# Kernel tuning notes

Measured on AMD Instinct MI355X. Metric: run time of the kernel, lower is better.

The kernel has to match this reference:

```python
import jax, jax.numpy as jnp
import numpy as np

LEVEL_SHAPES = ((100, 100), (50, 50), (25, 25))  # (H, W) per feature level
B, S, D, H, L, P, FFN = 2, 13125, 256, 8, 3, 4, 1024
Dh = D // H


def setup_inputs() -> dict:
    key = jax.random.key(0)
    ks = jax.random.split(key, 24)

    def rn(k, shape, s=0.02):
        return jax.random.normal(k, shape, jnp.float32) * s

    starts = np.cumsum([0] + [h * w for h, w in LEVEL_SHAPES])[:-1]
    return {
        "x": jax.random.normal(ks[0], (B, S, D), jnp.float32),
        "pos_embed": jax.random.normal(ks[1], (B, S, D), jnp.float32) * 0.1,
        "ref_points": jax.random.uniform(ks[2], (B, S, L, 2), jnp.float32),
        "W_off": rn(ks[3], (D, H * L * P * 2)),
        "b_off": rn(ks[4], (H * L * P * 2,), 0.5),
        "W_attn": rn(ks[5], (D, H * L * P)),
        "b_attn": rn(ks[6], (H * L * P,)),
        "W_val": rn(ks[7], (D, D)),
        "b_val": rn(ks[8], (D,)),
        "W_out": rn(ks[9], (D, D)),
        "b_out": rn(ks[10], (D,)),
        "g1": jnp.ones((D,), jnp.float32),
        "be1": jnp.zeros((D,), jnp.float32),
        "W1": rn(ks[11], (D, FFN)),
        "b1": rn(ks[12], (FFN,)),
        "W2": rn(ks[13], (FFN, D)),
        "b2": rn(ks[14], (D,)),
        "g2": jnp.ones((D,), jnp.float32),
        "be2": jnp.zeros((D,), jnp.float32),
        "level_shapes": jnp.array(LEVEL_SHAPES, jnp.int32),
        "level_start_idx": jnp.array(starts, jnp.int32),
    }


def layer_norm(x, g, b, eps=1e-5):
    m = jnp.mean(x, -1, keepdims=True)
    v = jnp.var(x, -1, keepdims=True)
    return (x - m) * jax.lax.rsqrt(v + eps) * g + b


def bilinear_sample(vl, loc, Hl, Wl):
    # vl: [B,H,S_l,Dh]; loc: [B,H,S,P,2] normalized (x,y) in [0,1]
    # grid_sample semantics: align_corners=False, padding_mode='zeros'
    x = loc[..., 0] * Wl - 0.5
    y = loc[..., 1] * Hl - 0.5
    x0 = jnp.floor(x)
    y0 = jnp.floor(y)
    fx = x - x0
    fy = y - y0
    x0i = x0.astype(jnp.int32)
    y0i = y0.astype(jnp.int32)
    out = 0.0
    for dy, dx, w in ((0, 0, (1 - fx) * (1 - fy)), (0, 1, fx * (1 - fy)),
                      (1, 0, (1 - fx) * fy), (1, 1, fx * fy)):
        xi = x0i + dx
        yi = y0i + dy
        valid = (xi >= 0) & (xi < Wl) & (yi >= 0) & (yi < Hl)
        idx = jnp.clip(yi, 0, Hl - 1) * Wl + jnp.clip(xi, 0, Wl - 1)
        b_, h_, s_, p_ = idx.shape
        g = jnp.take_along_axis(vl, idx.reshape(b_, h_, s_ * p_)[..., None], axis=2)
        g = g.reshape(b_, h_, s_, p_, Dh)
        out = out + g * (w * valid)[..., None]
    return out  # [B,H,S,P,Dh]


def ms_deform_attn(q, x, ref_points, W_off, b_off, W_attn, b_attn, W_val, b_val, W_out, b_out):
    value = (x @ W_val + b_val).reshape(B, S, H, Dh).transpose(0, 2, 1, 3)  # [B,H,S,Dh]
    off = (q @ W_off + b_off).reshape(B, S, H, L, P, 2)
    attn = jax.nn.softmax((q @ W_attn + b_attn).reshape(B, S, H, L * P), axis=-1)
    attn = attn.reshape(B, S, H, L, P).transpose(0, 2, 1, 3, 4)  # [B,H,S,L,P]
    # offset normalizer is (W, H) per level
    norm = jnp.array([[w, h] for h, w in LEVEL_SHAPES], jnp.float32)
    loc = ref_points[:, :, None, :, None, :] + off / norm[None, None, None, :, None, :]
    loc = loc.transpose(0, 2, 1, 3, 4, 5)  # [B,H,S,L,P,2]
    s0 = 0
    sampled = []
    for l, (Hl, Wl) in enumerate(LEVEL_SHAPES):
        vl = jax.lax.slice_in_dim(value, s0, s0 + Hl * Wl, axis=2)
        sampled.append(bilinear_sample(vl, loc[:, :, :, l], Hl, Wl))
        s0 += Hl * Wl
    sampled = jnp.stack(sampled, axis=3)  # [B,H,S,L,P,Dh]
    out = jnp.einsum('bhslp,bhslpd->bshd', attn, sampled).reshape(B, S, D)
    return out @ W_out + b_out


def reference(x, pos_embed, ref_points, W_off, b_off, W_attn, b_attn, W_val, b_val,
              W_out, b_out, g1, be1, W1, b1, W2, b2, g2, be2,
              level_shapes, level_start_idx):
    q = x + pos_embed
    attn_out = ms_deform_attn(q, x, ref_points, W_off, b_off, W_attn, b_attn,
                              W_val, b_val, W_out, b_out)
    h1 = layer_norm(x + attn_out, g1, be1)
    ffn = jax.nn.relu(h1 @ W1 + b1) @ W2 + b2
    return layer_norm(h1 + ffn, g2, be2)
```

## Files before the change

### kernel.cpp

```cpp
#include <hip/hip_runtime.h>
#include <hip/hip_bf16.h>

namespace {

constexpr int kB = 2, kS = 13125, kD = 256, kH = 8, kL = 3, kP = 4, kFFN = 1024, kDh = 32;
constexpr int kM = kB * kS;

typedef __attribute__((ext_vector_type(8))) short short8v;
typedef __attribute__((ext_vector_type(4))) float f32x4;
typedef __attribute__((ext_vector_type(2))) float f32x2;
typedef __attribute__((ext_vector_type(2))) unsigned int uint2v;

__device__ __forceinline__ float bf2f(unsigned short u) {
  unsigned int x = ((unsigned int)u) << 16;
  return __builtin_bit_cast(float, x);
}
__device__ __forceinline__ unsigned short f2bf(float f) {
  unsigned int u = __builtin_bit_cast(unsigned int, f);
  u += 0x7FFFu + ((u >> 16) & 1u);
  return (unsigned short)(u >> 16);
}

__device__ __forceinline__ void gload_lds16(const void* g, void* l) {
  __builtin_amdgcn_global_load_lds(
      (const __attribute__((address_space(1))) unsigned int*)g,
      (__attribute__((address_space(3))) unsigned int*)l, 16, 0, 0);
}

__global__ __launch_bounds__(256) void wprep_all(const float* __restrict__ Wv,
                                                 const float* __restrict__ Wo,
                                                 const float* __restrict__ Woff,
                                                 const float* __restrict__ Wattn,
                                                 const float* __restrict__ boff,
                                                 const float* __restrict__ battn,
                                                 const float* __restrict__ W1,
                                                 const float* __restrict__ W2,
                                                 unsigned short* __restrict__ Wvt,
                                                 unsigned short* __restrict__ Wot,
                                                 unsigned short* __restrict__ Wct,
                                                 float* __restrict__ bcomb,
                                                 unsigned short* __restrict__ W1t,
                                                 unsigned short* __restrict__ W2t) {
  int idx = blockIdx.x * 256 + threadIdx.x;
  if (idx < 65536) {
    int n = idx >> 8, k = idx & 255;
    Wvt[idx] = f2bf(Wv[k * 256 + n]);
  } else if (idx < 131072) {
    int j = idx - 65536;
    int n = j >> 8, k = j & 255;
    Wot[j] = f2bf(Wo[k * 256 + n]);
  } else if (idx < 204800) {
    int j = idx - 131072;
    int n = j >> 8, k = j & 255;
    int h = n / 36, jj = n - h * 36;
    float v = (jj < 24) ? Woff[(size_t)k * 192 + h * 24 + jj]
                        : Wattn[(size_t)k * 96 + h * 12 + (jj - 24)];
    Wct[j] = f2bf(v);
    if (j < 288) {
      int hh = j / 36, q = j - hh * 36;
      bcomb[j] = (q < 24) ? boff[hh * 24 + q] : battn[hh * 12 + (q - 24)];
    }
  } else if (idx < 466944) {
    int j = idx - 204800;
    int n = j >> 8, k = j & 255;
    W1t[j] = f2bf(W1[(size_t)k * 1024 + n]);
  } else if (idx < 729088) {
    int j = idx - 466944;
    int n = j >> 10, k = j & 1023;
    W2t[j] = f2bf(W2[(size_t)k * 256 + n]);
  }
}

__global__ __launch_bounds__(256) void prep_kernel(const float4* __restrict__ x,
                                                   const float4* __restrict__ pos,
                                                   ushort4* __restrict__ xb,
                                                   ushort4* __restrict__ qb, int n4) {
  int i = blockIdx.x * 256 + threadIdx.x;
  if (i < n4) {
    float4 a = x[i], b = pos[i];
    xb[i] = make_ushort4(f2bf(a.x), f2bf(a.y), f2bf(a.z), f2bf(a.w));
    qb[i] = make_ushort4(f2bf(a.x + b.x), f2bf(a.y + b.y),
                         f2bf(a.z + b.z), f2bf(a.w + b.w));
  }
}

template <int EPI, bool OBF, int MI, bool VHM>
__global__ __launch_bounds__(256) void mfma_gemm(const unsigned short* __restrict__ A,
                                                 const unsigned short* __restrict__ Bt,
                                                 const float* __restrict__ bias,
                                                 void* __restrict__ Cp,
                                                 int M, int N, int K) {
  constexpr int BM = MI * 32;
  __shared__ unsigned short smem[2 * 128 * 32];
  unsigned short* As = smem;
  unsigned short* Bs = smem + BM * 32;
  const int tid = threadIdx.x;
  const int w = tid >> 6, lane = tid & 63;
  const int m0 = blockIdx.y * BM, n0 = blockIdx.x * 128;
  const int wr = w >> 1, wc = w & 1;
  const int r_ = lane >> 2, sl = lane & 3;

  f32x4 acc[MI][4] = {};

  for (int k0 = 0; k0 < K; k0 += 32) {
#pragma unroll
    for (int i = 0; i < MI / 2; ++i) {
      const int row = i * 64 + w * 16 + r_;
      const int sg = sl ^ ((row >> 1) & 3);
      int arow = m0 + row;
      arow = arow < M ? arow : M - 1;
      gload_lds16(A + (size_t)arow * K + k0 + sg * 8, &As[(i * 64 + w * 16) * 32]);
    }
#pragma unroll
    for (int i = 0; i < 2; ++i) {
      const int row = i * 64 + w * 16 + r_;
      const int sg = sl ^ ((row >> 1) & 3);
      gload_lds16(Bt + (size_t)(n0 + row) * K + k0 + sg * 8, &Bs[(i * 64 + w * 16) * 32]);
    }
    __syncthreads();
    short8v a[MI], b[4];
#pragma unroll
    for (int mi = 0; mi < MI; ++mi) {
      const int row = wr * (MI * 16) + mi * 16 + (lane & 15);
      const int slot = (lane >> 4) ^ ((row >> 1) & 3);
      a[mi] = *(const short8v*)&As[row * 32 + slot * 8];
    }
#pragma unroll
    for (int ni = 0; ni < 4; ++ni) {
      const int row = wc * 64 + ni * 16 + (lane & 15);
      const int slot = (lane >> 4) ^ ((row >> 1) & 3);
      b[ni] = *(const short8v*)&Bs[row * 32 + slot * 8];
    }
#pragma unroll
    for (int mi = 0; mi < MI; ++mi)
#pragma unroll
      for (int ni = 0; ni < 4; ++ni)
        acc[mi][ni] = __builtin_amdgcn_mfma_f32_16x16x32_bf16(a[mi], b[ni], acc[mi][ni], 0, 0, 0);
    __syncthreads();
  }

  const int cr = lane >> 4, cc = lane & 15;
  if (OBF) {
    unsigned short* Cs = smem;
#pragma unroll
    for (int half = 0; half < MI / 2; ++half) {
      if (MI == 2 || wr == half) {
#pragma unroll
        for (int ni = 0; ni < 4; ++ni) {
          const int col = wc * 64 + ni * 16 + cc;
          const float bv = bias[n0 + col];
#pragma unroll
          for (int mi = 0; mi < MI; ++mi)
#pragma unroll
            for (int r = 0; r < 4; ++r) {
              const int loc = wr * (MI * 16) + mi * 16 + cr * 4 + r - half * 64;
              float v = acc[mi][ni][r] + bv;
              if (EPI == 2) v = fmaxf(v, 0.f);
              const int ch = (col >> 3) ^ (loc & 7);
              Cs[loc * 128 + ch * 8 + (col & 7)] = f2bf(v);
            }
        }
      }
      __syncthreads();
      const int lr = tid >> 4, lc = tid & 15;
#pragma unroll
      for (int pp = 0; pp < 4; ++pp) {
        const int loc = pp * 16 + lr;
        const int grow = m0 + half * 64 + loc;
        const short8v vv = *(const short8v*)&Cs[loc * 128 + ((lc ^ (loc & 7)) * 8)];
        if (grow < M) {
          if (VHM) {
            const int col = n0 + lc * 8;
            const int bb = grow >= kS ? 1 : 0;
            const int ss = grow - bb * kS;
            const int hh = col >> 5;
            *(short8v*)((unsigned short*)Cp +
                        (((size_t)(bb * kH + hh) * kS + ss) * kDh + (col & 31))) = vv;
          } else {
            *(short8v*)((unsigned short*)Cp + (size_t)grow * N + n0 + lc * 8) = vv;
          }
        }
      }
      __syncthreads();
    }
  } else {
#pragma unroll
    for (int ni = 0; ni < 4; ++ni) {
      const int col = n0 + wc * 64 + ni * 16 + cc;
      if (col >= N) continue;
      const float bv = bias[col];
#pragma unroll
      for (int mi = 0; mi < MI; ++mi) {
#pragma unroll
        for (int r = 0; r < 4; ++r) {
          const int row = m0 + wr * (MI * 16) + mi * 16 + cr * 4 + r;
          if (row >= M) continue;
          ((float*)Cp)[(size_t)row * N + col] = acc[mi][ni][r] + bv;
        }
      }
    }
  }
}

__global__ __launch_bounds__(256) void ffn_fused(const unsigned short* __restrict__ Ain,
                                                 const unsigned short* __restrict__ W1t,
                                                 const unsigned short* __restrict__ W2t,
                                                 const float* __restrict__ b1,
                                                 const float* __restrict__ b2,
                                                 unsigned short* __restrict__ Cp,
                                                 int M) {
  __shared__ unsigned short W1s[2][64 * 256];
  __shared__ unsigned short Ps[2 * 64 * 32];
  const int tid = threadIdx.x;
  const int w = tid >> 6, lane = tid & 63;
  const int m0 = blockIdx.x * 64;
  const int cr = lane >> 4, cc = lane & 15;

  short8v areg[8];
  {
    int grow = m0 + w * 16 + cc;
    grow = grow < M ? grow : M - 1;
    const unsigned short* ap = Ain + (size_t)grow * 256 + cr * 8;
#pragma unroll
    for (int kk = 0; kk < 8; ++kk) areg[kk] = *(const short8v*)(ap + kk * 32);
  }

  auto stage_w1 = [&](int jt, int buf) {
    const unsigned short* src = W1t + (size_t)jt * 64 * 256;
#pragma unroll
    for (int it = 0; it < 8; ++it) {
      const int idx = it * 256 + tid;
      const int kk = idx >> 8;
      const int row = (idx >> 2) & 63;
      const int sl = idx & 3;
      const int ssl = sl ^ ((row >> 1) & 3);
      gload_lds16(src + (size_t)row * 256 + kk * 32 + ssl * 8, &W1s[buf][idx * 8]);
    }
  };

  f32x4 acc[4][4] = {};

  stage_w1(0, 0);
  __syncthreads();

  for (int jt = 0; jt < 16; ++jt) {
    const int buf = jt & 1;
    if (jt < 15) stage_w1(jt + 1, buf ^ 1);

    short8v w2f[8];
#pragma unroll
    for (int kk2 = 0; kk2 < 2; ++kk2)
#pragma unroll
      for (int ni = 0; ni < 4; ++ni)
        w2f[kk2 * 4 + ni] = *(const short8v*)(W2t +
            (size_t)(w * 64 + ni * 16 + cc) * 1024 + jt * 64 + kk2 * 32 + cr * 8);

    f32x4 p1[4] = {};
#pragma unroll
    for (int kk = 0; kk < 8; ++kk) {
#pragma unroll
      for (int ni = 0; ni < 4; ++ni) {
        const int row = ni * 16 + cc;
        const short8v wv = *(const short8v*)
            &W1s[buf][kk * 2048 + row * 32 + ((cr ^ ((row >> 1) & 3)) * 8)];
        p1[ni] = __builtin_amdgcn_mfma_f32_16x16x32_bf16(wv, areg[kk], p1[ni], 0, 0, 0);
      }
    }
    {
      const int row = w * 16 + cc;
      const int rsw = (row >> 1) & 3;
#pragma unroll
      for (int ni = 0; ni < 4; ++ni) {
        const float4 bv = *(const float4*)&b1[jt * 64 + ni * 16 + cr * 4];
        const unsigned int u0 =
            (unsigned)f2bf(fmaxf(p1[ni][0] + bv.x, 0.f)) |
            ((unsigned)f2bf(fmaxf(p1[ni][1] + bv.y, 0.f)) << 16);
        const unsigned int u1 =
            (unsigned)f2bf(fmaxf(p1[ni][2] + bv.z, 0.f)) |
            ((unsigned)f2bf(fmaxf(p1[ni][3] + bv.w, 0.f)) << 16);
        const int kb = ni >> 1;
        const int slot = (ni & 1) * 2 + (cr >> 1);
        uint2v* dst = (uint2v*)&Ps[kb * 2048 + row * 32 + ((slot ^ rsw) * 8) + (cr & 1) * 4];
        *dst = (uint2v){u0, u1};
      }
    }
    __syncthreads();

#pragma unroll
    for (int kk2 = 0; kk2 < 2; ++kk2) {
      short8v pf[4];
#pragma unroll
      for (int mi = 0; mi < 4; ++mi) {
        const int row = mi * 16 + cc;
        pf[mi] = *(const short8v*)
            &Ps[kk2 * 2048 + row * 32 + ((cr ^ ((row >> 1) & 3)) * 8)];
      }
#pragma unroll
      for (int ni = 0; ni < 4; ++ni) {
#pragma unroll
        for (int mi = 0; mi < 4; ++mi)
          acc[mi][ni] = __builtin_amdgcn_mfma_f32_16x16x32_bf16(pf[mi], w2f[kk2 * 4 + ni],
                                                               acc[mi][ni], 0, 0, 0);
      }
    }
    __syncthreads();
  }

  unsigned short* Cs = &W1s[0][0];
#pragma unroll
  for (int ni = 0; ni < 4; ++ni) {
    const int col = w * 64 + ni * 16 + cc;
    const float bv = b2[col];
#pragma unroll
    for (int mi = 0; mi < 4; ++mi)
#pragma unroll
      for (int r = 0; r < 4; ++r) {
        const int row = mi * 16 + cr * 4 + r;
        const float v = acc[mi][ni][r] + bv;
        Cs[row * 256 + (((col >> 3) ^ (row & 7)) * 8) + (col & 7)] = f2bf(v);
      }
  }
  __syncthreads();
#pragma unroll
  for (int it = 0; it < 8; ++it) {
    const int row = it * 8 + (tid >> 5);
    const int grow = m0 + row;
    const int ch = tid & 31;
    const short8v vv = *(const short8v*)&Cs[row * 256 + ((ch ^ (row & 7)) * 8)];
    if (grow < M) *(short8v*)(Cp + (size_t)grow * 256 + ch * 8) = vv;
  }
}

__device__ __forceinline__ void acc2u(f32x2* acc, unsigned u, int i, float m) {
  f32x2 v;
  v.x = __builtin_bit_cast(float, u << 16);
  v.y = __builtin_bit_cast(float, u & 0xFFFF0000u);
  acc[i] += m * v;
}
__device__ __forceinline__ void acc_corner(f32x2* acc, uint4 q, float m) {
  acc2u(acc, q.x, 0, m);
  acc2u(acc, q.y, 1, m);
  acc2u(acc, q.z, 2, m);
  acc2u(acc, q.w, 3, m);
}

__global__ __launch_bounds__(256) void sample_kernel(const unsigned short* __restrict__ value,
                                                     const float* __restrict__ oa,
                                                     const float* __restrict__ refp,
                                                     unsigned short* __restrict__ out) {
  const int tid = threadIdx.x;
  const int sub = tid >> 2;
  const int lane = tid & 3;
  const int gi = blockIdx.x * 64 + sub;
  if (gi >= kB * kS * kH) return;
  const int h = gi & 7;
  const int bs = gi >> 3;
  const int b = (bs >= kS) ? 1 : 0;

  const float* op = oa + (size_t)bs * 288 + h * 36;
  const float* al = op + 24;
  float w[12];
  float mx = -1e30f;
#pragma unroll
  for (int i = 0; i < 12; ++i) { w[i] = al[i]; mx = fmaxf(mx, w[i]); }
  float sum = 0.f;
#pragma unroll
  for (int i = 0; i < 12; ++i) { w[i] = __expf(w[i] - mx); sum += w[i]; }
  const float inv = 1.f / sum;
#pragma unroll
  for (int i = 0; i < 12; ++i) w[i] *= inv;

  const float* rp = refp + (size_t)bs * (kL * 2);
  const unsigned short* vbase = value + ((size_t)(b * kH + h) * kS) * kDh + lane * 8;

  const int LH[3] = {100, 50, 25}, LW[3] = {100, 50, 25}, LS[3] = {0, 10000, 12500};
  f32x2 acc[4] = {};
#pragma unroll
  for (int l = 0; l < 3; ++l) {
    const int Wi = LW[l], Hi = LH[l];
    const float Wl = (float)Wi, Hl = (float)Hi;
    const float rxw = rp[l * 2 + 0] * Wl - 0.5f;
    const float ryh = rp[l * 2 + 1] * Hl - 0.5f;
    const unsigned short* lvl = vbase + (size_t)LS[l] * kDh;
#pragma unroll
    for (int p = 0; p < 4; ++p) {
      const float ox = op[l * 8 + p * 2 + 0], oy = op[l * 8 + p * 2 + 1];
      const float xf = rxw + ox;
      const float yf = ryh + oy;
      const float x0f = floorf(xf), y0f = floorf(yf);
      const float fx = xf - x0f, fy = yf - y0f;
      const int x0 = (int)x0f, y0 = (int)y0f;
      const int x1 = x0 + 1, y1 = y0 + 1;
      const bool vx0 = (unsigned)x0 < (unsigned)Wi;
      const bool vx1 = (unsigned)x1 < (unsigned)Wi;
      const bool vy0 = (unsigned)y0 < (unsigned)Hi;
      const bool vy1 = (unsigned)y1 < (unsigned)Hi;
      const int cx0 = min(max(x0, 0), Wi - 1), cx1 = min(max(x1, 0), Wi - 1);
      const int cy0 = min(max(y0, 0), Hi - 1), cy1 = min(max(y1, 0), Hi - 1);
      const float aw = w[l * 4 + p];
      const float ax = aw * fx, a0 = aw - ax;
      const float w00 = a0 - a0 * fy, w10 = a0 * fy;
      const float w01 = ax - ax * fy, w11 = ax * fy;
      const float m00 = (vx0 && vy0) ? w00 : 0.f;
      const float m01 = (vx1 && vy0) ? w01 : 0.f;
      const float m10 = (vx0 && vy1) ? w10 : 0.f;
      const float m11 = (vx1 && vy1) ? w11 : 0.f;
      const int ry0 = cy0 * Wi, ry1 = cy1 * Wi;
      const uint4 q00 = *(const uint4*)(lvl + (size_t)(ry0 + cx0) * kDh);
      const uint4 q01 = *(const uint4*)(lvl + (size_t)(ry0 + cx1) * kDh);
      const uint4 q10 = *(const uint4*)(lvl + (size_t)(ry1 + cx0) * kDh);
      const uint4 q11 = *(const uint4*)(lvl + (size_t)(ry1 + cx1) * kDh);
      acc_corner(acc, q00, m00);
      acc_corner(acc, q01, m01);
      acc_corner(acc, q10, m10);
      acc_corner(acc, q11, m11);
    }
  }
  unsigned short r[8];
#pragma unroll
  for (int i = 0; i < 4; ++i) {
    r[2 * i] = f2bf(acc[i].x);
    r[2 * i + 1] = f2bf(acc[i].y);
  }
  *(short8v*)(out + (size_t)bs * kD + h * kDh + lane * 8) = *(const short8v*)r;
}

template <int WB>
__global__ __launch_bounds__(256) void lnres_kernel(const float* __restrict__ X,
                                                    const unsigned short* __restrict__ Ab,
                                                    const float* __restrict__ g,
                                                    const float* __restrict__ be,
                                                    float* __restrict__ out,
                                                    unsigned short* __restrict__ outb,
                                                    int rows) {
  const int wid = threadIdx.x >> 6, lane = threadIdx.x & 63;
  const int row = blockIdx.x * 4 + wid;
  if (row >= rows) return;
  const float4 v = ((const float4*)(X + (size_t)row * kD))[lane];
  const ushort4 a4 = ((const ushort4*)(Ab + (size_t)row * kD))[lane];
  float4 t;
  t.x = v.x + bf2f(a4.x);
  t.y = v.y + bf2f(a4.y);
  t.z = v.z + bf2f(a4.z);
  t.w = v.w + bf2f(a4.w);
  float s = t.x + t.y + t.z + t.w;
  float sq = t.x * t.x + t.y * t.y + t.z * t.z + t.w * t.w;
#pragma unroll
  for (int o = 1; o < 64; o <<= 1) {
    s += __shfl_xor(s, o);
    sq += __shfl_xor(sq, o);
  }
  const float mean = s * (1.f / kD);
  const float var = sq * (1.f / kD) - mean * mean;
  const float rs = rsqrtf(var + 1e-5f);
  const float4 gg = ((const float4*)g)[lane];
  const float4 bb = ((const float4*)be)[lane];
  float4 o4;
  o4.x = (t.x - mean) * rs * gg.x + bb.x;
  o4.y = (t.y - mean) * rs * gg.y + bb.y;
  o4.z = (t.z - mean) * rs * gg.z + bb.z;
  o4.w = (t.w - mean) * rs * gg.w + bb.w;
  ((float4*)(out + (size_t)row * kD))[lane] = o4;
  if (WB) {
    ((ushort4*)(outb + (size_t)row * kD))[lane] =
        make_ushort4(f2bf(o4.x), f2bf(o4.y), f2bf(o4.z), f2bf(o4.w));
  }
}

}

extern "C" void kernel_launch(void* const* d_in, const int* in_sizes, int n_in,
                              void* d_out, int out_size, void* d_ws, size_t ws_size,
                              hipStream_t stream) {
  const float* x      = (const float*)d_in[0];
  const float* pos    = (const float*)d_in[1];
  const float* refp   = (const float*)d_in[2];
  const float* W_off  = (const float*)d_in[3];
  const float* b_off  = (const float*)d_in[4];
  const float* W_attn = (const float*)d_in[5];
  const float* b_attn = (const float*)d_in[6];
  const float* W_val  = (const float*)d_in[7];
  const float* b_val  = (const float*)d_in[8];
  const float* W_out  = (const float*)d_in[9];
  const float* b_out  = (const float*)d_in[10];
  const float* g1     = (const float*)d_in[11];
  const float* be1    = (const float*)d_in[12];
  const float* W1     = (const float*)d_in[13];
  const float* b1     = (const float*)d_in[14];
  const float* W2     = (const float*)d_in[15];
  const float* b2     = (const float*)d_in[16];
  const float* g2     = (const float*)d_in[17];
  const float* be2    = (const float*)d_in[18];
  float* outp = (float*)d_out;

  char* ws = (char*)d_ws;
  unsigned short* Wvt = (unsigned short*)(ws + 0);
  unsigned short* Wot = (unsigned short*)(ws + 131072);
  unsigned short* Wct = (unsigned short*)(ws + 262144);
  float* bcomb        = (float*)(ws + 262144 + 288 * 512);
  unsigned short* W1t = (unsigned short*)(ws + 458752);
  unsigned short* W2t = (unsigned short*)(ws + 983040);
  const size_t MDb = (size_t)kM * kD * 2;
  char* regA = ws + 1507328;
  char* regB = regA + MDb;
  char* regC = regB + MDb;
  char* regG = regC + 43680000;

  unsigned short* xb    = (unsigned short*)regA;
  unsigned short* aob   = (unsigned short*)regA;
  unsigned short* qb    = (unsigned short*)regB;
  unsigned short* f2b   = (unsigned short*)regB;
  unsigned short* value = (unsigned short*)regC;
  float* oa   = (float*)(regC + MDb);
  float* h1   = (float*)regC;
  unsigned short* h1b = (unsigned short*)(regC + (size_t)kM * kD * 4);
  unsigned short* sv  = (unsigned short*)regG;

  const dim3 blk(256);
  const int mt64 = (kM + 63) / 64;
  const int n4 = kM * kD / 4;

  wprep_all<<<(729088 + 255) / 256, blk, 0, stream>>>(W_val, W_out, W_off, W_attn,
                                                      b_off, b_attn, W1, W2,
                                                      Wvt, Wot, Wct, bcomb, W1t, W2t);
  prep_kernel<<<(n4 + 255) / 256, blk, 0, stream>>>((const float4*)x, (const float4*)pos,
                                                    (ushort4*)xb, (ushort4*)qb, n4);
  mfma_gemm<0, true, 2, true><<<dim3(2, mt64), blk, 0, stream>>>(xb, Wvt, b_val, value,
                                                                 kM, 256, 256);
  mfma_gemm<0, false, 2, false><<<dim3(3, mt64), blk, 0, stream>>>(qb, Wct, bcomb, oa,
                                                                   kM, 288, 256);
  sample_kernel<<<(kB * kS * kH + 63) / 64, blk, 0, stream>>>(value, oa, refp, sv);
  mfma_gemm<0, true, 2, false><<<dim3(2, mt64), blk, 0, stream>>>(sv, Wot, b_out, aob,
                                                                  kM, 256, 256);
  lnres_kernel<1><<<(kM + 3) / 4, blk, 0, stream>>>(x, aob, g1, be1, h1, h1b, kM);
  ffn_fused<<<mt64, blk, 0, stream>>>(h1b, W1t, W2t, b1, b2, f2b, kM);
  lnres_kernel<0><<<(kM + 3) / 4, blk, 0, stream>>>(h1, f2b, g2, be2, outp, nullptr, kM);
}
```

Measured before the change: 193.4 us.

## Fuse residual add and LayerNorm into output-projection and FFN GEMM epilogues

Replaces the out-projection GEMM plus the separate residual+LayerNorm kernel with one kernel that computes full 256-wide rows per 64-row block, adds the residual and reduces mean and variance across waves through LDS. The FFN kernel epilogue likewise adds the h1 residual and applies the second LayerNorm directly, writing the final fp32 output. This removes two launches and the bf16 round-trips of the attention output and FFN output. The residual and LN stats are now fp32 instead of bf16-rounded intermediates. The new GEMM reads B fragments straight from global memory without LDS staging, and the epilogues do scattered 4-byte stores.

Result: slower. 212.3 us (+9.8%).

```diff
diff --git a/kernel.cpp b/kernel.cpp
--- a/kernel.cpp
+++ b/kernel.cpp
@@ -202,12 +202,121 @@
   }
 }
 
+__global__ __launch_bounds__(256) void gemm_ln(const unsigned short* __restrict__ A,
+                                               const unsigned short* __restrict__ Bt,
+                                               const float* __restrict__ bias,
+                                               const float* __restrict__ R,
+                                               const float* __restrict__ g,
+                                               const float* __restrict__ be,
+                                               float* __restrict__ out,
+                                               unsigned short* __restrict__ outb,
+                                               int M) {
+  __shared__ unsigned short As[8 * 64 * 32];
+  __shared__ float red[4][64][2];
+  const int tid = threadIdx.x;
+  const int w = tid >> 6, lane = tid & 63;
+  const int m0 = blockIdx.x * 64;
+  const int cr = lane >> 4, cc = lane & 15;
+
+#pragma unroll
+  for (int it = 0; it < 8; ++it) {
+    const int idx = it * 256 + tid;
+    const int kk = idx >> 8;
+    const int row = (idx >> 2) & 63;
+    const int sl = idx & 3;
+    const int ssl = sl ^ ((row >> 1) & 3);
+    int grow = m0 + row;
+    grow = grow < M ? grow : M - 1;
+    gload_lds16(A + (size_t)grow * 256 + kk * 32 + ssl * 8, &As[idx * 8]);
+  }
+  __syncthreads();
+
+  f32x4 acc[4][4] = {};
+#pragma unroll
+  for (int kk = 0; kk < 8; ++kk) {
+    short8v pf[4];
+#pragma unroll
+    for (int mi = 0; mi < 4; ++mi) {
+      const int row = mi * 16 + cc;
+      pf[mi] = *(const short8v*)&As[kk * 2048 + row * 32 + ((cr ^ ((row >> 1) & 3)) * 8)];
+    }
+#pragma unroll
+    for (int ni = 0; ni < 4; ++ni) {
+      const short8v bW = *(const short8v*)(Bt +
+          (size_t)(w * 64 + ni * 16 + cc) * 256 + kk * 32 + cr * 8);
+#pragma unroll
+      for (int mi = 0; mi < 4; ++mi)
+        acc[mi][ni] = __builtin_amdgcn_mfma_f32_16x16x32_bf16(pf[mi], bW, acc[mi][ni], 0, 0, 0);
+    }
+  }
+
+  float bias4[4], gv[4], bev[4];
+#pragma unroll
+  for (int ni = 0; ni < 4; ++ni) {
+    const int col = w * 64 + ni * 16 + cc;
+    bias4[ni] = bias[col];
+    gv[ni] = g[col];
+    bev[ni] = be[col];
+  }
+#pragma unroll
+  for (int mi = 0; mi < 4; ++mi)
+#pragma unroll
+    for (int r = 0; r < 4; ++r) {
+      const int row = mi * 16 + cr * 4 + r;
+      const int grow = m0 + row;
+      float s = 0.f, q = 0.f;
+#pragma unroll
+      for (int ni = 0; ni < 4; ++ni) {
+        const int col = w * 64 + ni * 16 + cc;
+        float t = acc[mi][ni][r] + bias4[ni];
+        if (grow < M) t += R[(size_t)grow * 256 + col];
+        acc[mi][ni][r] = t;
+        s += t;
+        q += t * t;
+      }
+#pragma unroll
+      for (int o = 1; o < 16; o <<= 1) {
+        s += __shfl_xor(s, o);
+        q += __shfl_xor(q, o);
+      }
+      if (cc == 0) {
+        red[w][row][0] = s;
+        red[w][row][1] = q;
+      }
+    }
+  __syncthreads();
+#pragma unroll
+  for (int mi = 0; mi < 4; ++mi)
+#pragma unroll
+    for (int r = 0; r < 4; ++r) {
+      const int row = mi * 16 + cr * 4 + r;
+      const int grow = m0 + row;
+      const float s = red[0][row][0] + red[1][row][0] + red[2][row][0] + red[3][row][0];
+      const float q = red[0][row][1] + red[1][row][1] + red[2][row][1] + red[3][row][1];
+      const float mean = s * (1.f / 256.f);
+      const float var = q * (1.f / 256.f) - mean * mean;
+      const float rs = rsqrtf(var + 1e-5f);
+      if (grow < M) {
+#pragma unroll
+        for (int ni = 0; ni < 4; ++ni) {
+          const int col = w * 64 + ni * 16 + cc;
+          const float o = (acc[mi][ni][r] - mean) * rs * gv[ni] + bev[ni];
+          out[(size_t)grow * 256 + col] = o;
+          outb[(size_t)grow * 256 + col] = f2bf(o);
+        }
+      }
+    }
+}
+
 __global__ __launch_bounds__(256) void ffn_fused(const unsigned short* __restrict__ Ain,
                                                  const unsigned short* __restrict__ W1t,
                                                  const unsigned short* __restrict__ W2t,
                                                  const float* __restrict__ b1,
                                                  const float* __restrict__ b2,
-                                                 unsigned short* __restrict__ Cp,
+                                                 const float* __restrict__ H1,
+                                                 const float* __restrict__ g,
+                                                 const float* __restrict__ be,
+                                                 float* __restrict__ outp,
                                                  int M) {
   __shared__ unsigned short W1s[2][64 * 256];
   __shared__ unsigned short Ps[2 * 64 * 32];
@@ -306,29 +415,61 @@
     __syncthreads();
   }
 
-  unsigned short* Cs = &W1s[0][0];
+  float (*red)[2] = (float (*)[2])&Ps[0];
+  float bias4[4], gv[4], bev[4];
 #pragma unroll
   for (int ni = 0; ni < 4; ++ni) {
     const int col = w * 64 + ni * 16 + cc;
-    const float bv = b2[col];
-#pragma unroll
-    for (int mi = 0; mi < 4; ++mi)
-#pragma unroll
-      for (int r = 0; r < 4; ++r) {
-        const int row = mi * 16 + cr * 4 + r;
-        const float v = acc[mi][ni][r] + bv;
-        Cs[row * 256 + (((col >> 3) ^ (row & 7)) * 8) + (col & 7)] = f2bf(v);
-      }
-  }
+    bias4[ni] = b2[col];
+    gv[ni] = g[col];
+    bev[ni] = be[col];
+  }
+#pragma unroll
+  for (int mi = 0; mi < 4; ++mi)
+#pragma unroll
+    for (int r = 0; r < 4; ++r) {
+      const int row = mi * 16 + cr * 4 + r;
+      const int grow = m0 + row;
+      float s = 0.f, q = 0.f;
+#pragma unroll
+      for (int ni = 0; ni < 4; ++ni) {
+        const int col = w * 64 + ni * 16 + cc;
+        float t = acc[mi][ni][r] + bias4[ni];
+        if (grow < M) t += H1[(size_t)grow * 256 + col];
+        acc[mi][ni][r] = t;
+        s += t;
+        q += t * t;
+      }
+#pragma unroll
+      for (int o = 1; o < 16; o <<= 1) {
+        s += __shfl_xor(s, o);
+        q += __shfl_xor(q, o);
+      }
+      if (cc == 0) {
+        red[w * 64 + row][0] = s;
+        red[w * 64 + row][1] = q;
+      }
+    }
   __syncthreads();
 #pragma unroll
-  for (int it = 0; it < 8; ++it) {
-    const int row = it * 8 + (tid >> 5);
-    const int grow = m0 + row;
-    const int ch = tid & 31;
-    const short8v vv = *(const short8v*)&Cs[row * 256 + ((ch ^ (row & 7)) * 8)];
-    if (grow < M) *(short8v*)(Cp + (size_t)grow * 256 + ch * 8) = vv;
-  }
+  for (int mi = 0; mi < 4; ++mi)
+#pragma unroll
+    for (int r = 0; r < 4; ++r) {
+      const int row = mi * 16 + cr * 4 + r;
+      const int grow = m0 + row;
+      const float s = red[row][0] + red[64 + row][0] + red[128 + row][0] + red[192 + row][0];
+      const float q = red[row][1] + red[64 + row][1] + red[128 + row][1] + red[192 + row][1];
+      const float mean = s * (1.f / 256.f);
+      const float var = q * (1.f / 256.f) - mean * mean;
+      const float rs = rsqrtf(var + 1e-5f);
+      if (grow < M) {
+#pragma unroll
+        for (int ni = 0; ni < 4; ++ni) {
+          const int col = w * 64 + ni * 16 + cc;
+          outp[(size_t)grow * 256 + col] = (acc[mi][ni][r] - mean) * rs * gv[ni] + bev[ni];
+        }
+      }
+    }
 }
 
 __device__ __forceinline__ void acc2u(f32x2* acc, unsigned u, int i, float m) {
@@ -425,48 +566,6 @@
   *(short8v*)(out + (size_t)bs * kD + h * kDh + lane * 8) = *(const short8v*)r;
 }
 
-template <int WB>
-__global__ __launch_bounds__(256) void lnres_kernel(const float* __restrict__ X,
-                                                    const unsigned short* __restrict__ Ab,
-                                                    const float* __restrict__ g,
-                                                    const float* __restrict__ be,
-                                                    float* __restrict__ out,
-                                                    unsigned short* __restrict__ outb,
-                                                    int rows) {
-  const int wid = threadIdx.x >> 6, lane = threadIdx.x & 63;
-  const int row = blockIdx.x * 4 + wid;
-  if (row >= rows) return;
-  const float4 v = ((const float4*)(X + (size_t)row * kD))[lane];
-  const ushort4 a4 = ((const ushort4*)(Ab + (size_t)row * kD))[lane];
-  float4 t;
-  t.x = v.x + bf2f(a4.x);
-  t.y = v.y + bf2f(a4.y);
-  t.z = v.z + bf2f(a4.z);
-  t.w = v.w + bf2f(a4.w);
-  float s = t.x + t.y + t.z + t.w;
-  float sq = t.x * t.x + t.y * t.y + t.z * t.z + t.w * t.w;
-#pragma unroll
-  for (int o = 1; o < 64; o <<= 1) {
-    s += __shfl_xor(s, o);
-    sq += __shfl_xor(sq, o);
-  }
-  const float mean = s * (1.f / kD);
-  const float var = sq * (1.f / kD) - mean * mean;
-  const float rs = rsqrtf(var + 1e-5f);
-  const float4 gg = ((const float4*)g)[lane];
-  const float4 bb = ((const float4*)be)[lane];
-  float4 o4;
-  o4.x = (t.x - mean) * rs * gg.x + bb.x;
-  o4.y = (t.y - mean) * rs * gg.y + bb.y;
-  o4.z = (t.z - mean) * rs * gg.z + bb.z;
-  o4.w = (t.w - mean) * rs * gg.w + bb.w;
-  ((float4*)(out + (size_t)row * kD))[lane] = o4;
-  if (WB) {
-    ((ushort4*)(outb + (size_t)row * kD))[lane] =
-        make_ushort4(f2bf(o4.x), f2bf(o4.y), f2bf(o4.z), f2bf(o4.w));
-  }
-}
-
 }
 
 extern "C" void kernel_launch(void* const* d_in, const int* in_sizes, int n_in,
@@ -507,9 +606,7 @@
   char* regG = regC + 43680000;
 
   unsigned short* xb    = (unsigned short*)regA;
-  unsigned short* aob   = (unsigned short*)regA;
   unsigned short* qb    = (unsigned short*)regB;
-  unsigned short* f2b   = (unsigned short*)regB;
   unsigned short* value = (unsigned short*)regC;
   float* oa   = (float*)(regC + MDb);
   float* h1   = (float*)regC;
@@ -530,9 +627,6 @@
   mfma_gemm<0, false, 2, false><<<dim3(3, mt64), blk, 0, stream>>>(qb, Wct, bcomb, oa,
                                                                    kM, 288, 256);
   sample_kernel<<<(kB * kS * kH + 63) / 64, blk, 0, stream>>>(value, oa, refp, sv);
-  mfma_gemm<0, true, 2, false><<<dim3(2, mt64), blk, 0, stream>>>(sv, Wot, b_out, aob,
-                                                                  kM, 256, 256);
-  lnres_kernel<1><<<(kM + 3) / 4, blk, 0, stream>>>(x, aob, g1, be1, h1, h1b, kM);
-  ffn_fused<<<mt64, blk, 0, stream>>>(h1b, W1t, W2t, b1, b2, f2b, kM);
-  lnres_kernel<0><<<(kM + 3) / 4, blk, 0, stream>>>(h1, f2b, g2, be2, outp, nullptr, kM);
-}
+  gemm_ln<<<mt64, blk, 0, stream>>>(sv, Wot, b_out, x, g1, be1, h1, h1b, kM);
+  ffn_fused<<<mt64, blk, 0, stream>>>(h1b, W1t, W2t, b1, b2, h1, g2, be2, outp, kM);
+}
```
